# Kernel tuning notes

Measured on AMD Instinct MI355X. Metric: run time of the kernel, lower is better.

Reference implementation:

```python
import jax, jax.numpy as jnp
import numpy as np

B, S, D, H = 2, 2048, 2048, 16
HD = D // H  # head_dim = 128


def setup_inputs() -> dict:
    key = jax.random.key(0)
    ks = jax.random.split(key, 10)
    sc = 1.0 / np.sqrt(D)
    inp = {
        "hidden_states": jax.random.normal(ks[0], (B, S, D), dtype=jnp.float32),
        "attention_mask": jnp.zeros((B, 1, S, S), dtype=jnp.float32),
        "Wq": jax.random.normal(ks[1], (D, D), dtype=jnp.float32) * sc,
        "bq": jnp.zeros((D,), dtype=jnp.float32),
        "Wk": jax.random.normal(ks[2], (D, D), dtype=jnp.float32) * sc,
        "bk": jnp.zeros((D,), dtype=jnp.float32),
        "Wv": jax.random.normal(ks[3], (D, D), dtype=jnp.float32) * sc,
        "bv": jnp.zeros((D,), dtype=jnp.float32),
        "Wo": jax.random.normal(ks[4], (D, D), dtype=jnp.float32) * sc,
        "bo": jnp.zeros((D,), dtype=jnp.float32),
    }
    return inp


def reference(hidden_states, attention_mask, Wq, bq, Wk, bk, Wv, bv, Wo, bo):
    # torch Linear: y = x @ W^T + b
    q = hidden_states @ Wq.T + bq
    k = hidden_states @ Wk.T + bk
    v = hidden_states @ Wv.T + bv
    # [B,S,D] -> [B,H,S,HD]
    q = q.reshape(B, S, H, HD).transpose(0, 2, 1, 3)
    k = k.reshape(B, S, H, HD).transpose(0, 2, 1, 3)
    v = v.reshape(B, S, H, HD).transpose(0, 2, 1, 3)
    # RoPE in source is an identity passthrough; apply_rotary_pos_emb returns (q, k) unchanged.
    scores = jnp.einsum("bhqd,bhkd->bhqk", q, k) / jnp.sqrt(jnp.float32(HD))
    scores = scores + attention_mask  # broadcast over heads
    attn = jax.nn.softmax(scores, axis=-1)
    out = jnp.einsum("bhqk,bhkd->bhqd", attn, v)
    out = out.transpose(0, 2, 1, 3).reshape(B, S, D)
    return out @ Wo.T + bo
```

## Files before the change

### kernel.cpp

```cpp
#include <hip/hip_runtime.h>
#include <hip/hip_bf16.h>
#include <math.h>

typedef unsigned short u16;
typedef unsigned int u32;
typedef __attribute__((ext_vector_type(8))) short bf16x8;
typedef __attribute__((ext_vector_type(4))) float f32x4;

constexpr int Bc = 2, Sc = 2048, Dc = 2048, Hc = 16, HDc = 128;
constexpr int Mc = Bc * Sc;
constexpr float SCALE = 0.08838834764831845f;
constexpr float LOG2E = 1.4426950408889634f;

__device__ inline u16 f2bf(float f) {
  __hip_bfloat16 h = __float2bfloat16(f);
  return __builtin_bit_cast(u16, h);
}

typedef const __attribute__((address_space(1))) u32 glb_u32;
typedef __attribute__((address_space(3))) u32 lds_u32;
__device__ inline void gload16(const void* g, void* l) {
  __builtin_amdgcn_global_load_lds((glb_u32*)g, (lds_u32*)l, 16, 0, 0);
}

__global__ __launch_bounds__(256) void cvt5(
    const float* __restrict__ s0, u16* __restrict__ d0, int n0,
    const float* __restrict__ s1, u16* __restrict__ d1, int n1,
    const float* __restrict__ s2, u16* __restrict__ d2, int n2,
    const float* __restrict__ s3, u16* __restrict__ d3, int n3,
    const float* __restrict__ s4, u16* __restrict__ d4, int n4) {
  int i = blockIdx.x * 256 + threadIdx.x;
  const float* s; u16* d;
  if (i < n0) { s = s0; d = d0; }
  else { i -= n0;
    if (i < n1) { s = s1; d = d1; }
    else { i -= n1;
      if (i < n2) { s = s2; d = d2; }
      else { i -= n2;
        if (i < n3) { s = s3; d = d3; }
        else { i -= n3;
          if (i >= n4) return;
          s = s4; d = d4; } } } }
  float4 v = reinterpret_cast<const float4*>(s)[i];
  ushort4 o;
  o.x = f2bf(v.x); o.y = f2bf(v.y); o.z = f2bf(v.z); o.w = f2bf(v.w);
  reinterpret_cast<ushort4*>(d)[i] = o;
}

constexpr int GBM = 128, GBN = 128, GBK = 64;

__global__ __launch_bounds__(256) void qkv_gemm(
    const u16* __restrict__ A,
    const u16* __restrict__ Wq, const u16* __restrict__ Wk,
    const u16* __restrict__ Wv,
    const float* __restrict__ bq, const float* __restrict__ bk,
    const float* __restrict__ bv,
    u16* __restrict__ qout, u16* __restrict__ kout, u16* __restrict__ vout) {
  __shared__ u16 smem[17408];
  u16* As = smem;
  u16* Bs = smem + 8192;
  char* Asb = (char*)As;
  char* Bsb = (char*)Bs;
  const int t = threadIdx.x;
  const int w = t >> 6, lane = t & 63, g = lane >> 4, c = lane & 15;
  const int wm = w >> 1, wn = w & 1;
  const int m0 = blockIdx.y * GBM, n0 = blockIdx.x * GBN;
  const int z = blockIdx.z;
  const u16* W = (z == 0) ? Wq : (z == 1) ? Wk : Wv;
  const float* bias = (z == 0) ? bq : (z == 1) ? bk : bv;
  const float scale = (z == 0) ? SCALE * LOG2E : 1.0f;

  f32x4 acc[4][4];
#pragma unroll
  for (int m = 0; m < 4; ++m)
#pragma unroll
    for (int n = 0; n < 4; ++n) acc[m][n] = 0.f;

  for (int k0 = 0; k0 < Dc; k0 += GBK) {
#pragma unroll
    for (int i = 0; i < 4; ++i) {
      int u = i * 256 + t;
      int row = u >> 3, p = u & 7;
      int cu = (p ^ row) & 7;
      int ub = i * 256 + (t & 192);
      gload16(A + (size_t)(m0 + row) * Dc + k0 + cu * 8, Asb + ub * 16);
      gload16(W + (size_t)(n0 + row) * Dc + k0 + cu * 8, Bsb + ub * 16);
    }
    __syncthreads();
#pragma unroll
    for (int s = 0; s < 2; ++s) {
      bf16x8 af[4], bfv[4];
#pragma unroll
      for (int m = 0; m < 4; ++m) {
        int row = wm * 64 + m * 16 + c;
        int scu = ((s * 4 + g) ^ row) & 7;
        af[m] = *(const bf16x8*)(Asb + row * 128 + scu * 16);
      }
#pragma unroll
      for (int n = 0; n < 4; ++n) {
        int row = wn * 64 + n * 16 + c;
        int scu = ((s * 4 + g) ^ row) & 7;
        bfv[n] = *(const bf16x8*)(Bsb + row * 128 + scu * 16);
      }
#pragma unroll
      for (int m = 0; m < 4; ++m)
#pragma unroll
        for (int n = 0; n < 4; ++n)
          acc[m][n] = __builtin_amdgcn_mfma_f32_16x16x32_bf16(af[m], bfv[n], acc[m][n], 0, 0, 0);
    }
    __syncthreads();
  }

  if (z == 2) {
    u16* CT = smem;
    __syncthreads();
#pragma unroll
    for (int m = 0; m < 4; ++m)
#pragma unroll
      for (int n = 0; n < 4; ++n) {
        int lcol = wn * 64 + n * 16 + c;
        float bvv = bias[n0 + lcol];
#pragma unroll
        for (int r = 0; r < 4; ++r) {
          int lrow = wm * 64 + m * 16 + g * 4 + r;
          CT[lcol * 136 + lrow] = f2bf(acc[m][n][r] + bvv);
        }
      }
    __syncthreads();
    const int b = m0 >> 11, h = n0 >> 7, s0 = m0 & (Sc - 1);
#pragma unroll
    for (int i = 0; i < 8; ++i) {
      int u = i * 256 + t;
      int d = u >> 4, su = u & 15;
      size_t gbase = ((size_t)((b * Hc + h) * HDc) + d) * Sc + s0;
#pragma unroll
      for (int p2 = 0; p2 < 4; ++p2) {
        int sl = su * 8 + p2 * 2;
        u32 val = (u32)CT[d * 136 + sl] | ((u32)CT[d * 136 + sl + 1] << 16);
        int w6 = sl & 63, blk = sl >> 6;
        int slot = ((w6 >> 5) << 5) | (((w6 >> 2) & 3) << 3) |
                   (((w6 >> 4) & 1) << 2) | (w6 & 3);
        *(u32*)&vout[gbase + blk * 64 + slot] = val;
      }
    }
    return;
  }

  u16* outp = (z == 0) ? qout : kout;
#pragma unroll
  for (int m = 0; m < 4; ++m)
#pragma unroll
    for (int n = 0; n < 4; ++n) {
      int col = n0 + wn * 64 + n * 16 + c;
      float bvv = bias[col];
#pragma unroll
      for (int r = 0; r < 4; ++r) {
        int row = m0 + wm * 64 + m * 16 + g * 4 + r;
        float v = (acc[m][n][r] + bvv) * scale;
        int b = row >> 11, si = row & (Sc - 1);
        int h = col >> 7, d = col & (HDc - 1);
        outp[((size_t)((b * Hc + h) * Sc + si)) * HDc + d] = f2bf(v);
      }
    }
}

__global__ __launch_bounds__(256) void gemm_out(
    const u16* __restrict__ A, const u16* __restrict__ W,
    const float* __restrict__ bias, float* __restrict__ outp) {
  __shared__ u16 smem[16384];
  u16* As = smem;
  u16* Bs = smem + 8192;
  char* Asb = (char*)As;
  char* Bsb = (char*)Bs;
  const int t = threadIdx.x;
  const int w = t >> 6, lane = t & 63, g = lane >> 4, c = lane & 15;
  const int wm = w >> 1, wn = w & 1;
  const int m0 = blockIdx.y * GBM, n0 = blockIdx.x * GBN;

  f32x4 acc[4][4];
#pragma unroll
  for (int m = 0; m < 4; ++m)
#pragma unroll
    for (int n = 0; n < 4; ++n) acc[m][n] = 0.f;

  for (int k0 = 0; k0 < Dc; k0 += GBK) {
#pragma unroll
    for (int i = 0; i < 4; ++i) {
      int u = i * 256 + t;
      int row = u >> 3, p = u & 7;
      int cu = (p ^ row) & 7;
      int ub = i * 256 + (t & 192);
      gload16(A + (size_t)(m0 + row) * Dc + k0 + cu * 8, Asb + ub * 16);
      gload16(W + (size_t)(n0 + row) * Dc + k0 + cu * 8, Bsb + ub * 16);
    }
    __syncthreads();
#pragma unroll
    for (int s = 0; s < 2; ++s) {
      bf16x8 af[4], bfv[4];
#pragma unroll
      for (int m = 0; m < 4; ++m) {
        int row = wm * 64 + m * 16 + c;
        int scu = ((s * 4 + g) ^ row) & 7;
        af[m] = *(const bf16x8*)(Asb + row * 128 + scu * 16);
      }
#pragma unroll
      for (int n = 0; n < 4; ++n) {
        int row = wn * 64 + n * 16 + c;
        int scu = ((s * 4 + g) ^ row) & 7;
        bfv[n] = *(const bf16x8*)(Bsb + row * 128 + scu * 16);
      }
#pragma unroll
      for (int m = 0; m < 4; ++m)
#pragma unroll
        for (int n = 0; n < 4; ++n)
          acc[m][n] = __builtin_amdgcn_mfma_f32_16x16x32_bf16(af[m], bfv[n], acc[m][n], 0, 0, 0);
    }
    __syncthreads();
  }

#pragma unroll
  for (int m = 0; m < 4; ++m)
#pragma unroll
    for (int n = 0; n < 4; ++n) {
      int col = n0 + wn * 64 + n * 16 + c;
      float bv = bias[col];
#pragma unroll
      for (int r = 0; r < 4; ++r) {
        int row = m0 + wm * 64 + m * 16 + g * 4 + r;
        outp[(size_t)row * Dc + col] = acc[m][n][r] + bv;
      }
    }
}

__global__ __launch_bounds__(128, 2) void attn_mfma(
    const u16* __restrict__ Q, const u16* __restrict__ K,
    const u16* __restrict__ VT, const float* __restrict__ mask,
    u16* __restrict__ outb) {
  __shared__ u16 Ks[64 * 128];
  __shared__ u16 Vt[128 * 64];
  char* Ksb = (char*)Ks;
  char* Vtb = (char*)Vt;
  const int t = threadIdx.x, w = t >> 6, lane = t & 63, g = lane >> 4, c = lane & 15;
  const int bid = blockIdx.x;
  const int nid = (bid & 7) * 128 + (bid >> 3);
  const int bh = nid >> 5;
  const int q0 = (nid & 31) * 64;
  const int bq = bh >> 4, h = bh & 15;
  const u16* Qp = Q + ((size_t)bh << 18);
  const u16* Kp = K + ((size_t)bh << 18);
  const u16* VTp = VT + ((size_t)bh << 18);

  bf16x8 qf0[4], qf1[4];
  {
    int qr0 = q0 + w * 32 + c;
#pragma unroll
    for (int d0 = 0; d0 < 4; ++d0) {
      qf0[d0] = *(const bf16x8*)(Qp + (size_t)qr0 * HDc + d0 * 32 + g * 8);
      qf1[d0] = *(const bf16x8*)(Qp + (size_t)(qr0 + 16) * HDc + d0 * 32 + g * 8);
    }
  }

  f32x4 po0[8], po1[8];
#pragma unroll
  for (int m = 0; m < 8; ++m) { po0[m] = 0.f; po1[m] = 0.f; }
  float lsum0 = 0.f, lsum1 = 0.f;
  const float* mrow0 = mask + ((size_t)bq * Sc + q0 + w * 32 + c) * Sc;
  const float* mrow1 = mrow0 + (size_t)16 * Sc;

#pragma unroll 1
  for (int kt = 0; kt < 32; ++kt) {
    const int k0 = kt * 64;
#pragma unroll
    for (int i = 0; i < 8; ++i) {
      int u = i * 128 + t, row = u >> 4, p = u & 15;
      int cu = (p & 8) | ((p ^ row) & 7);
      gload16(Kp + (size_t)(k0 + row) * HDc + cu * 8,
              Ksb + (i * 128 + (t & 64)) * 16);
    }
#pragma unroll
    for (int i = 0; i < 8; ++i) {
      int u = i * 128 + t, d = u >> 3, p = u & 7;
      int cu = (p ^ d) & 7;
      gload16(VTp + (size_t)d * Sc + k0 + cu * 8,
              Vtb + (i * 128 + (t & 64)) * 16);
    }
    float4 mk0[4], mk1[4];
#pragma unroll
    for (int n = 0; n < 4; ++n) {
      mk0[n] = *(const float4*)(mrow0 + k0 + n * 16 + g * 4);
      mk1[n] = *(const float4*)(mrow1 + k0 + n * 16 + g * 4);
    }
    __syncthreads();

    f32x4 sfr0[4], sfr1[4];
#pragma unroll
    for (int n = 0; n < 4; ++n) { sfr0[n] = 0.f; sfr1[n] = 0.f; }
    __builtin_amdgcn_s_setprio(1);
#pragma unroll
    for (int ds = 0; ds < 4; ++ds)
#pragma unroll
      for (int n = 0; n < 4; ++n) {
        int row = n * 16 + c;
        int cu = ds * 4 + g;
        int scu = (cu & 8) | ((cu ^ row) & 7);
        bf16x8 kf = *(const bf16x8*)(Ksb + row * 256 + scu * 16);
        sfr0[n] = __builtin_amdgcn_mfma_f32_16x16x32_bf16(kf, qf0[ds], sfr0[n], 0, 0, 0);
        sfr1[n] = __builtin_amdgcn_mfma_f32_16x16x32_bf16(kf, qf1[ds], sfr1[n], 0, 0, 0);
      }
    __builtin_amdgcn_s_setprio(0);

    u32 a01[4], a23[4], b01[4], b23[4];
#pragma unroll
    for (int n = 0; n < 4; ++n) {
      float p0 = __builtin_amdgcn_exp2f(fmaf(mk0[n].x, LOG2E, sfr0[n][0]));
      float p1 = __builtin_amdgcn_exp2f(fmaf(mk0[n].y, LOG2E, sfr0[n][1]));
      float p2 = __builtin_amdgcn_exp2f(fmaf(mk0[n].z, LOG2E, sfr0[n][2]));
      float p3 = __builtin_amdgcn_exp2f(fmaf(mk0[n].w, LOG2E, sfr0[n][3]));
      lsum0 += (p0 + p1) + (p2 + p3);
      a01[n] = (u32)f2bf(p0) | ((u32)f2bf(p1) << 16);
      a23[n] = (u32)f2bf(p2) | ((u32)f2bf(p3) << 16);
      float r0 = __builtin_amdgcn_exp2f(fmaf(mk1[n].x, LOG2E, sfr1[n][0]));
      float r1 = __builtin_amdgcn_exp2f(fmaf(mk1[n].y, LOG2E, sfr1[n][1]));
      float r2 = __builtin_amdgcn_exp2f(fmaf(mk1[n].z, LOG2E, sfr1[n][2]));
      float r3 = __builtin_amdgcn_exp2f(fmaf(mk1[n].w, LOG2E, sfr1[n][3]));
      lsum1 += (r0 + r1) + (r2 + r3);
      b01[n] = (u32)f2bf(r0) | ((u32)f2bf(r1) << 16);
      b23[n] = (u32)f2bf(r2) | ((u32)f2bf(r3) << 16);
    }

    __builtin_amdgcn_s_setprio(1);
#pragma unroll
    for (int s2 = 0; s2 < 2; ++s2) {
      uint4 pw0, pw1;
      pw0.x = a01[s2 * 2]; pw0.y = a23[s2 * 2];
      pw0.z = a01[s2 * 2 + 1]; pw0.w = a23[s2 * 2 + 1];
      pw1.x = b01[s2 * 2]; pw1.y = b23[s2 * 2];
      pw1.z = b01[s2 * 2 + 1]; pw1.w = b23[s2 * 2 + 1];
      bf16x8 pf0 = __builtin_bit_cast(bf16x8, pw0);
      bf16x8 pf1 = __builtin_bit_cast(bf16x8, pw1);
#pragma unroll
      for (int m = 0; m < 8; ++m) {
        int d = m * 16 + c;
        int scuv = ((s2 * 4 + g) ^ (d & 7)) & 7;
        bf16x8 vf = *(const bf16x8*)(Vtb + d * 128 + scuv * 16);
        po0[m] = __builtin_amdgcn_mfma_f32_16x16x32_bf16(vf, pf0, po0[m], 0, 0, 0);
        po1[m] = __builtin_amdgcn_mfma_f32_16x16x32_bf16(vf, pf1, po1[m], 0, 0, 0);
      }
    }
    __builtin_amdgcn_s_setprio(0);
    __syncthreads();
  }

  lsum0 += __shfl_xor(lsum0, 16, 64);
  lsum0 += __shfl_xor(lsum0, 32, 64);
  lsum1 += __shfl_xor(lsum1, 16, 64);
  lsum1 += __shfl_xor(lsum1, 32, 64);
  const float rl0 = 1.0f / lsum0;
  const float rl1 = 1.0f / lsum1;
  const int qg0 = q0 + w * 32 + c;
  u16* ob0 = outb + ((size_t)(bq * Sc + qg0)) * Dc + h * HDc;
  u16* ob1 = ob0 + (size_t)16 * Dc;
#pragma unroll
  for (int m = 0; m < 8; ++m) {
    ushort4 o4;
    o4.x = f2bf(po0[m][0] * rl0);
    o4.y = f2bf(po0[m][1] * rl0);
    o4.z = f2bf(po0[m][2] * rl0);
    o4.w = f2bf(po0[m][3] * rl0);
    *(ushort4*)(ob0 + m * 16 + g * 4) = o4;
    ushort4 o5;
    o5.x = f2bf(po1[m][0] * rl1);
    o5.y = f2bf(po1[m][1] * rl1);
    o5.z = f2bf(po1[m][2] * rl1);
    o5.w = f2bf(po1[m][3] * rl1);
    *(ushort4*)(ob1 + m * 16 + g * 4) = o5;
  }
}

extern "C" void kernel_launch(void* const* d_in, const int* in_sizes, int n_in,
                              void* d_out, int out_size, void* d_ws,
                              size_t ws_size, hipStream_t stream) {
  const float* hs   = (const float*)d_in[0];
  const float* mask = (const float*)d_in[1];
  const float* Wq   = (const float*)d_in[2];
  const float* bqp  = (const float*)d_in[3];
  const float* Wk   = (const float*)d_in[4];
  const float* bkp  = (const float*)d_in[5];
  const float* Wv   = (const float*)d_in[6];
  const float* bvp  = (const float*)d_in[7];
  const float* Wo   = (const float*)d_in[8];
  const float* bop  = (const float*)d_in[9];

  u16* Xb  = (u16*)d_ws;
  u16* Wqb = Xb + (size_t)Mc * Dc;
  u16* Wkb = Wqb + (size_t)Dc * Dc;
  u16* Wvb = Wkb + (size_t)Dc * Dc;
  u16* Wob = Wvb + (size_t)Dc * Dc;
  u16* qb  = Wob + (size_t)Dc * Dc;
  u16* kb  = qb + (size_t)Mc * Dc;
  u16* vtb = kb + (size_t)Mc * Dc;
  u16* ab  = vtb + (size_t)Mc * Dc;

  const int nh4 = Mc * Dc / 4;
  const int nw4 = Dc * Dc / 4;
  cvt5<<<dim3((nh4 + 4 * nw4) / 256), dim3(256), 0, stream>>>(
      hs, Xb, nh4, Wq, Wqb, nw4, Wk, Wkb, nw4, Wv, Wvb, nw4, Wo, Wob, nw4);

  qkv_gemm<<<dim3(Dc / GBN, Mc / GBM, 3), dim3(256), 0, stream>>>(
      Xb, Wqb, Wkb, Wvb, bqp, bkp, bvp, qb, kb, vtb);
  attn_mfma<<<dim3(1024), dim3(128), 0, stream>>>(qb, kb, vtb, mask, ab);
  gemm_out<<<dim3(Dc / GBN, Mc / GBM), dim3(256), 0, stream>>>(
      ab, Wob, bop, (float*)d_out);
}
```

Before: 301.8 us.

## Split QKV projection into a double-buffered 256x256-tile Q/K GEMM and separate V GEMM

Replaces the fused 128x128-tile QKV GEMM with two kernels. Q and K now use a new 512-thread kernel with 256x256 output tiles, a double-buffered LDS pipeline that prefetches the next K-slice while computing the current one, explicit vmcnt waits and raised MFMA priority. V keeps the original 128x128 kernel and its transposed epilogue. The aim is more data reuse per tile and hiding global-load latency behind compute, at the cost of an extra launch, 128KB of LDS per block (one block per CU) and a Q/K grid of exactly 256 blocks, which could leave CUs idle.

```diff
diff --git a/kernel.cpp b/kernel.cpp
--- a/kernel.cpp
+++ b/kernel.cpp
@@ -47,15 +47,123 @@
   reinterpret_cast<ushort4*>(d)[i] = o;
 }
 
+__global__ __launch_bounds__(512, 2) void qk_gemm8(
+    const u16* __restrict__ A, const u16* __restrict__ Wq,
+    const u16* __restrict__ Wk, const float* __restrict__ bq,
+    const float* __restrict__ bk, u16* __restrict__ qout,
+    u16* __restrict__ kout) {
+  __shared__ u16 lds[65536];
+  char* L = (char*)lds;
+  const int t = threadIdx.x, w = t >> 6, lane = t & 63, g = lane >> 4, c = lane & 15;
+  const int wm = w >> 2, wn = w & 3;
+  const int m0 = blockIdx.y * 256, n0 = blockIdx.x * 256;
+  const int z = blockIdx.z;
+  const u16* W = z ? Wk : Wq;
+  const float* bias = z ? bk : bq;
+  const float scale = z ? 1.0f : SCALE * LOG2E;
+
+  f32x4 acc[8][4];
+#pragma unroll
+  for (int m = 0; m < 8; ++m)
+#pragma unroll
+    for (int n = 0; n < 4; ++n) acc[m][n] = 0.f;
+
+  const u16* sPtr[8];
+  int dOff[8];
+#pragma unroll
+  for (int i = 0; i < 8; ++i) {
+    int i2 = i & 3;
+    int u = i2 * 512 + t;
+    int row = u >> 3, p = u & 7;
+    int cu = (p ^ row) & 7;
+    const u16* base = (i < 4) ? (A + (size_t)(m0 + row) * Dc)
+                              : (W + (size_t)(n0 + row) * Dc);
+    sPtr[i] = base + cu * 8;
+    dOff[i] = ((i >= 4) ? 32768 : 0) + (i2 >> 1) * 16384 +
+              ((i2 & 1) * 512 + (t & 448)) * 16;
+  }
+
+  auto STAGE = [&](int d) {
+#pragma unroll
+    for (int i = 0; i < 8; ++i) {
+      gload16(sPtr[i], L + d * 65536 + dOff[i]);
+      sPtr[i] += 64;
+    }
+  };
+
+  STAGE(0);
+  asm volatile("s_waitcnt vmcnt(0)" ::: "memory");
+  asm volatile("s_barrier" ::: "memory");
+
+  int cur = 0;
+  const char* AbBase = L + wm * 16384;
+  const char* BbBase = L + 32768 + (wn >> 1) * 16384;
+  const int rB0 = (wn & 1) * 64;
+
+#pragma unroll 1
+  for (int s = 0; s < 32; ++s) {
+    if (s + 1 < 32) {
+      STAGE(cur ^ 1);
+      asm volatile("s_waitcnt vmcnt(8)" ::: "memory");
+    } else {
+      asm volatile("s_waitcnt vmcnt(0)" ::: "memory");
+    }
+    asm volatile("s_barrier" ::: "memory");
+
+    const char* Ab = AbBase + cur * 65536;
+    const char* Bb = BbBase + cur * 65536;
+#pragma unroll
+    for (int mh = 0; mh < 2; ++mh)
+#pragma unroll
+      for (int ks = 0; ks < 2; ++ks) {
+        bf16x8 af[4], bf[4];
+#pragma unroll
+        for (int m4 = 0; m4 < 4; ++m4) {
+          int row = (mh * 4 + m4) * 16 + c;
+          af[m4] = *(const bf16x8*)(Ab + row * 128 + (((ks * 4 + g) ^ row) & 7) * 16);
+        }
+#pragma unroll
+        for (int n = 0; n < 4; ++n) {
+          int row = rB0 + n * 16 + c;
+          bf[n] = *(const bf16x8*)(Bb + row * 128 + (((ks * 4 + g) ^ row) & 7) * 16);
+        }
+        __builtin_amdgcn_s_setprio(1);
+#pragma unroll
+        for (int m4 = 0; m4 < 4; ++m4)
+#pragma unroll
+          for (int n = 0; n < 4; ++n)
+            acc[mh * 4 + m4][n] =
+                __builtin_amdgcn_mfma_f32_16x16x32_bf16(af[m4], bf[n], acc[mh * 4 + m4][n], 0, 0, 0);
+        __builtin_amdgcn_s_setprio(0);
+      }
+
+    asm volatile("s_barrier" ::: "memory");
+    cur ^= 1;
+  }
+
+  u16* outp = z ? kout : qout;
+#pragma unroll
+  for (int n = 0; n < 4; ++n) {
+    int col = n0 + wn * 64 + n * 16 + c;
+    float bvv = bias[col];
+    int h = col >> 7, d = col & (HDc - 1);
+#pragma unroll
+    for (int m = 0; m < 8; ++m)
+#pragma unroll
+      for (int r = 0; r < 4; ++r) {
+        int row = m0 + wm * 128 + m * 16 + g * 4 + r;
+        int b = row >> 11, si = row & (Sc - 1);
+        outp[((size_t)((b * Hc + h) * Sc + si)) * HDc + d] =
+            f2bf((acc[m][n][r] + bvv) * scale);
+      }
+  }
+}
+
 constexpr int GBM = 128, GBN = 128, GBK = 64;
 
-__global__ __launch_bounds__(256) void qkv_gemm(
-    const u16* __restrict__ A,
-    const u16* __restrict__ Wq, const u16* __restrict__ Wk,
-    const u16* __restrict__ Wv,
-    const float* __restrict__ bq, const float* __restrict__ bk,
-    const float* __restrict__ bv,
-    u16* __restrict__ qout, u16* __restrict__ kout, u16* __restrict__ vout) {
+__global__ __launch_bounds__(256) void v_gemm(
+    const u16* __restrict__ A, const u16* __restrict__ W,
+    const float* __restrict__ bias, u16* __restrict__ vout) {
   __shared__ u16 smem[17408];
   u16* As = smem;
   u16* Bs = smem + 8192;
@@ -65,10 +173,6 @@
   const int w = t >> 6, lane = t & 63, g = lane >> 4, c = lane & 15;
   const int wm = w >> 1, wn = w & 1;
   const int m0 = blockIdx.y * GBM, n0 = blockIdx.x * GBN;
-  const int z = blockIdx.z;
-  const u16* W = (z == 0) ? Wq : (z == 1) ? Wk : Wv;
-  const float* bias = (z == 0) ? bq : (z == 1) ? bk : bv;
-  const float scale = (z == 0) ? SCALE * LOG2E : 1.0f;
 
   f32x4 acc[4][4];
 #pragma unroll
@@ -111,57 +215,37 @@
     __syncthreads();
   }
 
-  if (z == 2) {
-    u16* CT = smem;
-    __syncthreads();
-#pragma unroll
-    for (int m = 0; m < 4; ++m)
-#pragma unroll
-      for (int n = 0; n < 4; ++n) {
-        int lcol = wn * 64 + n * 16 + c;
-        float bvv = bias[n0 + lcol];
-#pragma unroll
-        for (int r = 0; r < 4; ++r) {
-          int lrow = wm * 64 + m * 16 + g * 4 + r;
-          CT[lcol * 136 + lrow] = f2bf(acc[m][n][r] + bvv);
-        }
-      }
-    __syncthreads();
-    const int b = m0 >> 11, h = n0 >> 7, s0 = m0 & (Sc - 1);
-#pragma unroll
-    for (int i = 0; i < 8; ++i) {
-      int u = i * 256 + t;
-      int d = u >> 4, su = u & 15;
-      size_t gbase = ((size_t)((b * Hc + h) * HDc) + d) * Sc + s0;
-#pragma unroll
-      for (int p2 = 0; p2 < 4; ++p2) {
-        int sl = su * 8 + p2 * 2;
-        u32 val = (u32)CT[d * 136 + sl] | ((u32)CT[d * 136 + sl + 1] << 16);
-        int w6 = sl & 63, blk = sl >> 6;
-        int slot = ((w6 >> 5) << 5) | (((w6 >> 2) & 3) << 3) |
-                   (((w6 >> 4) & 1) << 2) | (w6 & 3);
-        *(u32*)&vout[gbase + blk * 64 + slot] = val;
-      }
-    }
-    return;
-  }
-
-  u16* outp = (z == 0) ? qout : kout;
+  u16* CT = smem;
+  __syncthreads();
 #pragma unroll
   for (int m = 0; m < 4; ++m)
 #pragma unroll
     for (int n = 0; n < 4; ++n) {
-      int col = n0 + wn * 64 + n * 16 + c;
-      float bvv = bias[col];
+      int lcol = wn * 64 + n * 16 + c;
+      float bvv = bias[n0 + lcol];
 #pragma unroll
       for (int r = 0; r < 4; ++r) {
-        int row = m0 + wm * 64 + m * 16 + g * 4 + r;
-        float v = (acc[m][n][r] + bvv) * scale;
-        int b = row >> 11, si = row & (Sc - 1);
-        int h = col >> 7, d = col & (HDc - 1);
-        outp[((size_t)((b * Hc + h) * Sc + si)) * HDc + d] = f2bf(v);
-      }
-    }
+        int lrow = wm * 64 + m * 16 + g * 4 + r;
+        CT[lcol * 136 + lrow] = f2bf(acc[m][n][r] + bvv);
+      }
+    }
+  __syncthreads();
+  const int b = m0 >> 11, h = n0 >> 7, s0 = m0 & (Sc - 1);
+#pragma unroll
+  for (int i = 0; i < 8; ++i) {
+    int u = i * 256 + t;
+    int d = u >> 4, su = u & 15;
+    size_t gbase = ((size_t)((b * Hc + h) * HDc) + d) * Sc + s0;
+#pragma unroll
+    for (int p2 = 0; p2 < 4; ++p2) {
+      int sl = su * 8 + p2 * 2;
+      u32 val = (u32)CT[d * 136 + sl] | ((u32)CT[d * 136 + sl + 1] << 16);
+      int w6 = sl & 63, blk = sl >> 6;
+      int slot = ((w6 >> 5) << 5) | (((w6 >> 2) & 3) << 3) |
+                 (((w6 >> 4) & 1) << 2) | (w6 & 3);
+      *(u32*)&vout[gbase + blk * 64 + slot] = val;
+    }
+  }
 }
 
 __global__ __launch_bounds__(256) void gemm_out(
@@ -406,8 +490,10 @@
   cvt5<<<dim3((nh4 + 4 * nw4) / 256), dim3(256), 0, stream>>>(
       hs, Xb, nh4, Wq, Wqb, nw4, Wk, Wkb, nw4, Wv, Wvb, nw4, Wo, Wob, nw4);
 
-  qkv_gemm<<<dim3(Dc / GBN, Mc / GBM, 3), dim3(256), 0, stream>>>(
-      Xb, Wqb, Wkb, Wvb, bqp, bkp, bvp, qb, kb, vtb);
+  qk_gemm8<<<dim3(Dc / 256, Mc / 256, 2), dim3(512), 0, stream>>>(
+      Xb, Wqb, Wkb, bqp, bkp, qb, kb);
+  v_gemm<<<dim3(Dc / GBN, Mc / GBM), dim3(256), 0, stream>>>(
+      Xb, Wvb, bvp, vtb);
   attn_mfma<<<dim3(1024), dim3(128), 0, stream>>>(qb, kb, vtb, mask, ab);
   gemm_out<<<dim3(Dc / GBN, Mc / GBM), dim3(256), 0, stream>>>(
       ab, Wob, bop, (float*)d_out);
```

After: 289.5 us. -4.1%, faster.
